# Kernel tuning notes

Hardware: AMD Instinct MI355X
Metric: run time of the kernel (lower is better)

Reference implementation:

```python
import jax, jax.numpy as jnp
import numpy as np

D_MODEL = 768
N_HEADS = 12
D_HEAD = D_MODEL // N_HEADS


def setup_inputs() -> dict:
    key = jax.random.key(0)
    k_x, k_qw, k_qb, k_ow, k_ob = jax.random.split(key, 5)
    B, N = 2, 4096
    scale = 1.0 / np.sqrt(D_MODEL)
    return {
        "x": jax.random.normal(k_x, (B, N, D_MODEL), dtype=jnp.float32),
        # torch nn.Linear stores weight as [out_features, in_features]
        "qkv_w": jax.random.uniform(k_qw, (3 * D_MODEL, D_MODEL), jnp.float32, -scale, scale),
        "qkv_b": jax.random.uniform(k_qb, (3 * D_MODEL,), jnp.float32, -scale, scale),
        "out_w": jax.random.uniform(k_ow, (D_MODEL, D_MODEL), jnp.float32, -scale, scale),
        "out_b": jax.random.uniform(k_ob, (D_MODEL,), jnp.float32, -scale, scale),
    }


def reference(x, qkv_w, qkv_b, out_w, out_b):
    B, N, D = x.shape
    qkv = x @ qkv_w.T + qkv_b                                   # [B, N, 3D]
    qkv = qkv.reshape(B, N, 3, N_HEADS, D_HEAD)
    qkv = jnp.transpose(qkv, (2, 0, 3, 1, 4))                    # [3, B, H, N, d]
    q, k, v = qkv[0], qkv[1], qkv[2]
    scores = jnp.einsum("bhqd,bhkd->bhqk", q, k) / np.sqrt(D_HEAD)
    attn = jax.nn.softmax(scores, axis=-1)
    out = jnp.einsum("bhqk,bhkd->bhqd", attn, v)                 # [B, H, N, d]
    out = jnp.transpose(out, (0, 2, 1, 3)).reshape(B, N, D)
    return out @ out_w.T + out_b
```

## Files before the change

### kernel.cpp

```cpp
#include <hip/hip_runtime.h>
#include <cstdint>

#define SEQ 4096
#define NH 12
#define DH 64
#define DM 768
#define MT 8192
#define QKVN 2304

typedef __bf16 bf16;
typedef __attribute__((ext_vector_type(8))) __bf16 bf16x8;
typedef __attribute__((ext_vector_type(4))) __bf16 bf16x4;
typedef __attribute__((ext_vector_type(2))) __bf16 bf16x2;
typedef __attribute__((ext_vector_type(4))) float f32x4;
typedef __attribute__((ext_vector_type(16))) float f32x16;
typedef __attribute__((ext_vector_type(2))) int int2v;

__device__ __forceinline__ void async_ld16(const void* g, void* lds) {
  __builtin_amdgcn_global_load_lds(
      (__attribute__((address_space(1))) void*)(void*)g,
      (__attribute__((address_space(3))) void*)lds, 16, 0, 0);
}

__device__ __forceinline__ int sexp2_bits(float s) {
  return (int)__builtin_fmaf(s, 8388608.0f, 1065091072.0f);
}

__device__ __forceinline__ int pack_hi16(int lo, int hi) {
#if __has_builtin(__builtin_amdgcn_perm)
  return (int)__builtin_amdgcn_perm((unsigned)hi, (unsigned)lo, 0x07060302u);
#else
  return (int)(((unsigned)lo >> 16) | ((unsigned)hi & 0xffff0000u));
#endif
}

__device__ __forceinline__ void lane32_swap(int& a, int& b) {
#if __has_builtin(__builtin_amdgcn_permlane32_swap)
  int2v r = __builtin_amdgcn_permlane32_swap(a, b, false, false);
  a = r.x; b = r.y;
#else
  int hi = (threadIdx.x & 63) >> 5;
  int ra = __shfl_xor(a, 32, 64), rb = __shfl_xor(b, 32, 64);
  int na = hi ? rb : a;
  int nb = hi ? b : ra;
  a = na; b = nb;
#endif
}

#define NX4  (MT * DM / 4)
#define NW14 (QKVN * DM / 4)
#define NW24 (DM * DM / 4)
__global__ void cvt_all(const float* __restrict__ x, const float* __restrict__ w1,
                        const float* __restrict__ w2, bf16* __restrict__ xb,
                        bf16* __restrict__ wb1, bf16* __restrict__ wb2) {
  int i = blockIdx.x * blockDim.x + threadIdx.x;
  const float* src; bf16* dst; int j;
  if (i < NX4) { src = x; dst = xb; j = i; }
  else if (i < NX4 + NW14) { src = w1; dst = wb1; j = i - NX4; }
  else if (i < NX4 + NW14 + NW24) { src = w2; dst = wb2; j = i - NX4 - NW14; }
  else return;
  f32x4 v = ((const f32x4*)src)[j];
  bf16x4 o;
  o.x = (bf16)v.x; o.y = (bf16)v.y; o.z = (bf16)v.z; o.w = (bf16)v.w;
  ((bf16x4*)dst)[j] = o;
}

template<int MODE>
__global__ __launch_bounds__(256) void gemm_bt(
    const bf16* __restrict__ A, const bf16* __restrict__ Bw,
    const float* __restrict__ bias,
    bf16* __restrict__ outQ, bf16* __restrict__ outK, bf16* __restrict__ outVt,
    float* __restrict__ outF,
    int M, int N, int K)
{
  __shared__ bf16 smem[2 * 128 * 64];
  bf16* sA = smem;
  bf16* sB = smem + 128 * 64;
  bf16* sT = smem;

  const int tid  = threadIdx.x;
  const int wave = tid >> 6;
  const int lane = tid & 63;
  const int l15  = lane & 15;
  const int quad = lane >> 4;

  constexpr int NT = (MODE == 0) ? (QKVN / 128) : (DM / 128);
  const int lin = blockIdx.x;
  const int rem = lin % (NT * 8);
  const int m0 = ((lin / (NT * 8)) * 8 + (rem % 8)) * 128;
  const int n0 = (rem / 8) * 128;

  const int rowbase = (wave >> 1) * 64;
  const int colbase = (wave & 1) * 64;

  f32x4 acc[4][4] = {};

  const int srow = lane >> 3;
  const int spg  = (lane & 7) ^ srow;
  const int xk   = l15 & 7;

  for (int kt = 0; kt < K; kt += 64) {
#pragma unroll
    for (int p = 0; p < 8; ++p) {
      int chunk = p * 4 + wave;
      if (chunk < 16) {
        int row = chunk * 8 + srow;
        async_ld16(A + (size_t)(m0 + row) * K + kt + spg * 8, &sA[chunk * 512]);
      } else {
        int row = (chunk - 16) * 8 + srow;
        async_ld16(Bw + (size_t)(n0 + row) * K + kt + spg * 8, &sB[(chunk - 16) * 512]);
      }
    }
    __syncthreads();

#pragma unroll
    for (int ks = 0; ks < 2; ++ks) {
      bf16x8 af[4], bfr[4];
#pragma unroll
      for (int rt = 0; rt < 4; ++rt)
        af[rt] = *(const bf16x8*)&sA[(rowbase + rt * 16 + l15) * 64 +
                                     (((ks * 4 + quad) ^ xk) * 8)];
#pragma unroll
      for (int ct = 0; ct < 4; ++ct)
        bfr[ct] = *(const bf16x8*)&sB[(colbase + ct * 16 + l15) * 64 +
                                      (((ks * 4 + quad) ^ xk) * 8)];
#pragma unroll
      for (int rt = 0; rt < 4; ++rt)
#pragma unroll
        for (int ct = 0; ct < 4; ++ct)
          acc[rt][ct] = __builtin_amdgcn_mfma_f32_16x16x32_bf16(af[rt], bfr[ct], acc[rt][ct], 0, 0, 0);
    }
    __syncthreads();
  }

  if (MODE == 0) {
    const int g = n0 / DM;
    if (g < 2) {
      const float qscale = 0.125f * 1.4426950408889634f;
#pragma unroll
      for (int ct = 0; ct < 4; ++ct) {
        int j = n0 + colbase + ct * 16 + l15;
        float bj = bias[j];
        int f = j % DM;
        int h = f >> 6, d = f & 63;
#pragma unroll
        for (int rt = 0; rt < 4; ++rt) {
          int mrow = m0 + rowbase + rt * 16 + quad * 4;
#pragma unroll
          for (int r = 0; r < 4; ++r) {
            float v = acc[rt][ct][r] + bj;
            int m = mrow + r;
            int b = m >> 12, n = m & 4095;
            int bh = b * NH + h;
            if (g == 0) outQ[((size_t)bh * SEQ + n) * DH + d] = (bf16)(v * qscale);
            else        outK[((size_t)bh * SEQ + n) * DH + d] = (bf16)v;
          }
        }
      }
    } else {
      const int f0 = n0 - 2 * DM;
      const int b = m0 >> 12, n0m = m0 & 4095;
#pragma unroll
      for (int p = 0; p < 2; ++p) {
        __syncthreads();
        if (colbase == p * 64) {
#pragma unroll
          for (int ct = 0; ct < 4; ++ct) {
            int jl = ct * 16 + l15;
            float bj = bias[n0 + p * 64 + jl];
#pragma unroll
            for (int rt = 0; rt < 4; ++rt) {
              int ml = rowbase + rt * 16 + quad * 4;
#pragma unroll
              for (int r = 0; r < 4; ++r)
                sT[jl * 136 + ml + r] = (bf16)(acc[rt][ct][r] + bj);
            }
          }
        }
        __syncthreads();
#pragma unroll
        for (int p2 = 0; p2 < 4; ++p2) {
          int slot = p2 * 256 + tid;
          int jr = slot >> 4, mc = (slot & 15) * 8;
          int fj = f0 + p * 64 + jr;
          int h = fj >> 6, d = fj & 63;
          *(bf16x8*)&outVt[((size_t)(b * NH + h) * DH + d) * SEQ + n0m + mc] =
              *(const bf16x8*)&sT[jr * 136 + mc];
        }
      }
    }
  } else {
#pragma unroll
    for (int ct = 0; ct < 4; ++ct) {
      int j = n0 + colbase + ct * 16 + l15;
      float bj = bias[j];
#pragma unroll
      for (int rt = 0; rt < 4; ++rt) {
        int mrow = m0 + rowbase + rt * 16 + quad * 4;
#pragma unroll
        for (int r = 0; r < 4; ++r)
          outF[(size_t)(mrow + r) * N + j] = acc[rt][ct][r] + bj;
      }
    }
  }
}

#define SOFTPV(S, R0, R1, R2, R3, OA, OB) do {                               \
    int b0 = sexp2_bits(S[8*kc+0]); int b1 = sexp2_bits(S[8*kc+1]);          \
    int b2 = sexp2_bits(S[8*kc+2]); int b3 = sexp2_bits(S[8*kc+3]);          \
    int b4 = sexp2_bits(S[8*kc+4]); int b5 = sexp2_bits(S[8*kc+5]);          \
    int b6 = sexp2_bits(S[8*kc+6]); int b7 = sexp2_bits(S[8*kc+7]);          \
    R0 += __int_as_float(b0 & 0xffff0000) + __int_as_float(b4 & 0xffff0000); \
    R1 += __int_as_float(b1 & 0xffff0000) + __int_as_float(b5 & 0xffff0000); \
    R2 += __int_as_float(b2 & 0xffff0000) + __int_as_float(b6 & 0xffff0000); \
    R3 += __int_as_float(b3 & 0xffff0000) + __int_as_float(b7 & 0xffff0000); \
    int g0a = pack_hi16(b0, b1), g0b = pack_hi16(b2, b3);                    \
    int g1a = pack_hi16(b4, b5), g1b = pack_hi16(b6, b7);                    \
    lane32_swap(g0a, g1a); lane32_swap(g0b, g1b);                            \
    union { int i[4]; bf16x8 v; } Af_;                                       \
    Af_.i[0] = g0a; Af_.i[1] = g0b; Af_.i[2] = g1a; Af_.i[3] = g1b;          \
    OA = __builtin_amdgcn_mfma_f32_32x32x16_bf16(Af_.v, vf0, OA, 0, 0, 0);   \
    OB = __builtin_amdgcn_mfma_f32_32x32x16_bf16(Af_.v, vf1, OB, 0, 0, 0);   \
  } while (0)

__global__ __launch_bounds__(256, 2) void flash_attn(
    const bf16* __restrict__ Q, const bf16* __restrict__ Kg,
    const bf16* __restrict__ Vt, bf16* __restrict__ Oout)
{
  __shared__ bf16 sK[2][64 * 64];
  __shared__ bf16 sV[2][64 * 64];

  const int L    = blockIdx.x + (SEQ / 256) * blockIdx.y;
  const int xcd  = L & 7;
  const int slot = L >> 3;
  const int bh   = xcd + 8 * (slot >> 4);
  const int qb   = slot & 15;

  {
    int ph = (qb + bh) & 3;
    if (ph == 1) __builtin_amdgcn_s_sleep(2);
    else if (ph == 2) __builtin_amdgcn_s_sleep(4);
    else if (ph == 3) __builtin_amdgcn_s_sleep(6);
  }

  const int tid  = threadIdx.x;
  const int wave = tid >> 6;
  const int lane = tid & 63;
  const int l31  = lane & 31;
  const int hi   = lane >> 5;
  const int q0w  = qb * 256 + wave * 64;

  const bf16* Qb = Q  + (size_t)bh * SEQ * DH;
  const bf16* Kb = Kg + (size_t)bh * SEQ * DH;
  const bf16* Vb = Vt + (size_t)bh * DH * SEQ;

  const int srow = lane >> 3;
  const int spg  = lane & 7;

  bf16x8 qf0[4], qf1[4];
#pragma unroll
  for (int dc = 0; dc < 4; ++dc) {
    qf0[dc] = *(const bf16x8*)&Qb[(size_t)(q0w + l31) * DH + dc * 16 + hi * 8];
    qf1[dc] = *(const bf16x8*)&Qb[(size_t)(q0w + 32 + l31) * DH + dc * 16 + hi * 8];
  }

  f32x16 o00 = {}, o01 = {}, o10 = {}, o11 = {};
  float r00 = 0.f, r01 = 0.f, r02 = 0.f, r03 = 0.f;
  float r10 = 0.f, r11 = 0.f, r12 = 0.f, r13 = 0.f;

  const int keyk = (l31 & 7) ^ (((l31 >> 3) & 3) << 1);
  int off[4];
#pragma unroll
  for (int dc = 0; dc < 4; ++dc)
    off[dc] = l31 * 64 + (((dc * 2 + hi) ^ keyk) * 8);

  auto stage = [&](int kt, int buf) {
#pragma unroll
    for (int j = 0; j < 2; ++j) {
      int r0 = wave * 16 + j * 8;
      int row = r0 + srow;
      int lg = spg ^ (row & 7) ^ (((row >> 3) & 3) << 1);
      async_ld16(Kb + (size_t)(kt + row) * DH + lg * 8, &sK[buf][r0 * 64]);
      async_ld16(Vb + (size_t)row * SEQ + kt + lg * 8, &sV[buf][r0 * 64]);
    }
  };

  auto compute = [&](const bf16* sKp, const bf16* sVp) {
#pragma unroll
    for (int kb = 0; kb < 2; ++kb) {
      bf16x8 kf[4];
#pragma unroll
      for (int dc = 0; dc < 4; ++dc)
        kf[dc] = *(const bf16x8*)&sKp[off[dc] + kb * 2048];
      f32x16 s0 = {}, s1 = {};
#pragma unroll
      for (int dc = 0; dc < 4; ++dc) {
        s0 = __builtin_amdgcn_mfma_f32_32x32x16_bf16(kf[dc], qf0[dc], s0, 0, 0, 0);
        s1 = __builtin_amdgcn_mfma_f32_32x32x16_bf16(kf[dc], qf1[dc], s1, 0, 0, 0);
      }
#pragma unroll
      for (int kc = 0; kc < 2; ++kc) {
        bf16x8 vf0 = *(const bf16x8*)&sVp[off[kb * 2 + kc]];
        bf16x8 vf1 = *(const bf16x8*)&sVp[off[kb * 2 + kc] + 2048];
        SOFTPV(s0, r00, r01, r02, r03, o00, o01);
        SOFTPV(s1, r10, r11, r12, r13, o10, o11);
      }
    }
  };

  stage(0, 0);
  __syncthreads();

  for (int kt = 0; kt < SEQ; kt += 128) {
    if (kt + 64 < SEQ) stage(kt + 64, 1);
    compute(sK[0], sV[0]);
    __syncthreads();
    if (kt + 128 < SEQ) stage(kt + 128, 0);
    compute(sK[1], sV[1]);
    __syncthreads();
  }

  float rsum0 = (r00 + r01) + (r02 + r03);
  rsum0 += __shfl_xor(rsum0, 32, 64);
  float inv0 = 1.0f / rsum0;
  float rsum1 = (r10 + r11) + (r12 + r13);
  rsum1 += __shfl_xor(rsum1, 32, 64);
  float inv1 = 1.0f / rsum1;

  const int bg = bh / NH, h = bh % NH;
#pragma unroll
  for (int i = 0; i < 16; ++i) {
    int ql = 8 * (i >> 2) + (i & 3) + 4 * hi;
    float iva = __shfl(inv0, ql, 64);
    size_t basea = (size_t)(bg * SEQ + q0w + ql) * DM + h * DH;
    Oout[basea + l31]      = (bf16)(o00[i] * iva);
    Oout[basea + 32 + l31] = (bf16)(o01[i] * iva);
    float ivb = __shfl(inv1, ql, 64);
    size_t baseb = (size_t)(bg * SEQ + q0w + 32 + ql) * DM + h * DH;
    Oout[baseb + l31]      = (bf16)(o10[i] * ivb);
    Oout[baseb + 32 + l31] = (bf16)(o11[i] * ivb);
  }
}

extern "C" void kernel_launch(void* const* d_in, const int* in_sizes, int n_in,
                              void* d_out, int out_size, void* d_ws, size_t ws_size,
                              hipStream_t stream) {
  const float* x     = (const float*)d_in[0];
  const float* qkv_w = (const float*)d_in[1];
  const float* qkv_b = (const float*)d_in[2];
  const float* out_w = (const float*)d_in[3];
  const float* out_b = (const float*)d_in[4];
  float* out = (float*)d_out;

  char* w = (char*)d_ws;
  bf16* xb    = (bf16*)w; w += (size_t)MT * DM * 2;
  bf16* wqkv  = (bf16*)w; w += (size_t)QKVN * DM * 2;
  bf16* wout  = (bf16*)w; w += (size_t)DM * DM * 2;
  bf16* Qw    = (bf16*)w; w += (size_t)MT * DM * 2;
  bf16* Kw    = (bf16*)w; w += (size_t)MT * DM * 2;
  bf16* Vtw   = (bf16*)w; w += (size_t)MT * DM * 2;
  bf16* attnV = (bf16*)w; w += (size_t)MT * DM * 2;

  const int tot4 = NX4 + NW14 + NW24;
  cvt_all<<<dim3((tot4 + 255) / 256), 256, 0, stream>>>(x, qkv_w, out_w, xb, wqkv, wout);

  gemm_bt<0><<<dim3((QKVN / 128) * (MT / 128)), 256, 0, stream>>>(
      xb, wqkv, qkv_b, Qw, Kw, Vtw, nullptr, MT, QKVN, DM);

  flash_attn<<<dim3(SEQ / 256, 2 * NH), 256, 0, stream>>>(Qw, Kw, Vtw, attnV);

  gemm_bt<1><<<dim3((DM / 128) * (MT / 128)), 256, 0, stream>>>(
      attnV, wout, out_b, nullptr, nullptr, nullptr, out, MT, DM, DM);
}
```

Measured before the change: 283.8 us.

## Split attention key range in two with fp32 partials and a merge kernel

Flash attention now splits each query block's key sequence into two halves, doubling the grid from 384 to 768 blocks. Each half writes unnormalized fp32 outputs and row sums to workspace, and a new merge kernel adds them, normalizes and writes bf16. Launch bounds move to 3 blocks per CU and the first QK MFMA starts from a constant zero accumulator. This trades extra global traffic (about 50MB of fp32 partials) and one more launch for better CU occupancy and load balance. The old path remains as a fallback when the workspace is too small.

```diff
diff --git a/kernel.cpp b/kernel.cpp
--- a/kernel.cpp
+++ b/kernel.cpp
@@ -7,6 +7,7 @@
 #define DM 768
 #define MT 8192
 #define QKVN 2304
+#define BH 24
 
 typedef __bf16 bf16;
 typedef __attribute__((ext_vector_type(8))) __bf16 bf16x8;
@@ -223,21 +224,32 @@
     OB = __builtin_amdgcn_mfma_f32_32x32x16_bf16(Af_.v, vf1, OB, 0, 0, 0);   \
   } while (0)
 
-__global__ __launch_bounds__(256, 2) void flash_attn(
+template<int SPLIT>
+__global__ __launch_bounds__(256, 3) void flash_attn(
     const bf16* __restrict__ Q, const bf16* __restrict__ Kg,
-    const bf16* __restrict__ Vt, bf16* __restrict__ Oout)
+    const bf16* __restrict__ Vt, float* __restrict__ Op,
+    float* __restrict__ Rs, bf16* __restrict__ Oout)
 {
   __shared__ bf16 sK[2][64 * 64];
   __shared__ bf16 sV[2][64 * 64];
 
-  const int L    = blockIdx.x + (SEQ / 256) * blockIdx.y;
-  const int xcd  = L & 7;
-  const int slot = L >> 3;
-  const int bh   = xcd + 8 * (slot >> 4);
-  const int qb   = slot & 15;
+  int bh, qb, kh;
+  if (SPLIT) {
+    const int L    = blockIdx.x + 32 * blockIdx.y;
+    const int slot = L >> 3;
+    bh = (L & 7) + 8 * (slot >> 5);
+    qb = (slot & 31) >> 1;
+    kh = slot & 1;
+  } else {
+    const int L    = blockIdx.x + 16 * blockIdx.y;
+    const int slot = L >> 3;
+    bh = (L & 7) + 8 * (slot >> 4);
+    qb = slot & 15;
+    kh = 0;
+  }
 
   {
-    int ph = (qb + bh) & 3;
+    int ph = (qb + bh + kh) & 3;
     if (ph == 1) __builtin_amdgcn_s_sleep(2);
     else if (ph == 2) __builtin_amdgcn_s_sleep(4);
     else if (ph == 3) __builtin_amdgcn_s_sleep(6);
@@ -249,6 +261,8 @@
   const int l31  = lane & 31;
   const int hi   = lane >> 5;
   const int q0w  = qb * 256 + wave * 64;
+  const int kbase = SPLIT ? kh * (SEQ / 2) : 0;
+  const int kend  = SPLIT ? kbase + SEQ / 2 : SEQ;
 
   const bf16* Qb = Q  + (size_t)bh * SEQ * DH;
   const bf16* Kb = Kg + (size_t)bh * SEQ * DH;
@@ -265,6 +279,7 @@
   }
 
   f32x16 o00 = {}, o01 = {}, o10 = {}, o11 = {};
+  const f32x16 zc = {};
   float r00 = 0.f, r01 = 0.f, r02 = 0.f, r03 = 0.f;
   float r10 = 0.f, r11 = 0.f, r12 = 0.f, r13 = 0.f;
 
@@ -292,9 +307,10 @@
 #pragma unroll
       for (int dc = 0; dc < 4; ++dc)
         kf[dc] = *(const bf16x8*)&sKp[off[dc] + kb * 2048];
-      f32x16 s0 = {}, s1 = {};
-#pragma unroll
-      for (int dc = 0; dc < 4; ++dc) {
+      f32x16 s0 = __builtin_amdgcn_mfma_f32_32x32x16_bf16(kf[0], qf0[0], zc, 0, 0, 0);
+      f32x16 s1 = __builtin_amdgcn_mfma_f32_32x32x16_bf16(kf[0], qf1[0], zc, 0, 0, 0);
+#pragma unroll
+      for (int dc = 1; dc < 4; ++dc) {
         s0 = __builtin_amdgcn_mfma_f32_32x32x16_bf16(kf[dc], qf0[dc], s0, 0, 0, 0);
         s1 = __builtin_amdgcn_mfma_f32_32x32x16_bf16(kf[dc], qf1[dc], s1, 0, 0, 0);
       }
@@ -308,38 +324,75 @@
     }
   };
 
-  stage(0, 0);
+  stage(kbase, 0);
   __syncthreads();
 
-  for (int kt = 0; kt < SEQ; kt += 128) {
-    if (kt + 64 < SEQ) stage(kt + 64, 1);
+  for (int kt = kbase; kt < kend; kt += 128) {
+    if (kt + 64 < kend) stage(kt + 64, 1);
     compute(sK[0], sV[0]);
     __syncthreads();
-    if (kt + 128 < SEQ) stage(kt + 128, 0);
+    if (kt + 128 < kend) stage(kt + 128, 0);
     compute(sK[1], sV[1]);
     __syncthreads();
   }
 
   float rsum0 = (r00 + r01) + (r02 + r03);
   rsum0 += __shfl_xor(rsum0, 32, 64);
-  float inv0 = 1.0f / rsum0;
   float rsum1 = (r10 + r11) + (r12 + r13);
   rsum1 += __shfl_xor(rsum1, 32, 64);
-  float inv1 = 1.0f / rsum1;
-
-  const int bg = bh / NH, h = bh % NH;
-#pragma unroll
-  for (int i = 0; i < 16; ++i) {
-    int ql = 8 * (i >> 2) + (i & 3) + 4 * hi;
-    float iva = __shfl(inv0, ql, 64);
-    size_t basea = (size_t)(bg * SEQ + q0w + ql) * DM + h * DH;
-    Oout[basea + l31]      = (bf16)(o00[i] * iva);
-    Oout[basea + 32 + l31] = (bf16)(o01[i] * iva);
-    float ivb = __shfl(inv1, ql, 64);
-    size_t baseb = (size_t)(bg * SEQ + q0w + 32 + ql) * DM + h * DH;
-    Oout[baseb + l31]      = (bf16)(o10[i] * ivb);
-    Oout[baseb + 32 + l31] = (bf16)(o11[i] * ivb);
-  }
+
+  if (SPLIT) {
+    float* Oh = Op + ((size_t)(kh * BH + bh) * SEQ + q0w) * DH;
+    if (hi == 0) {
+      float* Rh = Rs + (size_t)(kh * BH + bh) * SEQ + q0w;
+      Rh[l31]      = rsum0;
+      Rh[32 + l31] = rsum1;
+    }
+#pragma unroll
+    for (int i = 0; i < 16; ++i) {
+      int ql = 8 * (i >> 2) + (i & 3) + 4 * hi;
+      Oh[(size_t)ql * DH + l31]             = o00[i];
+      Oh[(size_t)ql * DH + 32 + l31]        = o01[i];
+      Oh[(size_t)(32 + ql) * DH + l31]      = o10[i];
+      Oh[(size_t)(32 + ql) * DH + 32 + l31] = o11[i];
+    }
+  } else {
+    float inv0 = 1.0f / rsum0;
+    float inv1 = 1.0f / rsum1;
+    const int bg = bh / NH, h = bh % NH;
+#pragma unroll
+    for (int i = 0; i < 16; ++i) {
+      int ql = 8 * (i >> 2) + (i & 3) + 4 * hi;
+      float iva = __shfl(inv0, ql, 64);
+      size_t basea = (size_t)(bg * SEQ + q0w + ql) * DM + h * DH;
+      Oout[basea + l31]      = (bf16)(o00[i] * iva);
+      Oout[basea + 32 + l31] = (bf16)(o01[i] * iva);
+      float ivb = __shfl(inv1, ql, 64);
+      size_t baseb = (size_t)(bg * SEQ + q0w + 32 + ql) * DM + h * DH;
+      Oout[baseb + l31]      = (bf16)(o10[i] * ivb);
+      Oout[baseb + 32 + l31] = (bf16)(o11[i] * ivb);
+    }
+  }
+}
+
+__global__ __launch_bounds__(256) void merge_halves(
+    const float* __restrict__ Op, const float* __restrict__ Rs,
+    bf16* __restrict__ attnV)
+{
+  int i = blockIdx.x * 256 + threadIdx.x;
+  if (i >= BH * SEQ * (DH / 4)) return;
+  int dq = i & 15, row = i >> 4;
+  f32x4 a = ((const f32x4*)Op)[(size_t)row * 16 + dq];
+  f32x4 b = ((const f32x4*)Op)[((size_t)BH * SEQ + row) * 16 + dq];
+  float inv = 1.0f / (Rs[row] + Rs[BH * SEQ + row]);
+  int q = row & (SEQ - 1), bh = row >> 12;
+  int bg = bh / NH, h = bh % NH;
+  bf16x4 r;
+  r.x = (bf16)((a.x + b.x) * inv);
+  r.y = (bf16)((a.y + b.y) * inv);
+  r.z = (bf16)((a.z + b.z) * inv);
+  r.w = (bf16)((a.w + b.w) * inv);
+  *(bf16x4*)&attnV[((size_t)(bg * SEQ + q)) * DM + h * DH + dq * 4] = r;
 }
 
 extern "C" void kernel_launch(void* const* d_in, const int* in_sizes, int n_in,
@@ -360,6 +413,9 @@
   bf16* Kw    = (bf16*)w; w += (size_t)MT * DM * 2;
   bf16* Vtw   = (bf16*)w; w += (size_t)MT * DM * 2;
   bf16* attnV = (bf16*)w; w += (size_t)MT * DM * 2;
+  float* Opf  = (float*)w; w += (size_t)2 * BH * SEQ * DH * 4;
+  float* Rsf  = (float*)w; w += (size_t)2 * BH * SEQ * 4;
+  const size_t ws_need = (size_t)(w - (char*)d_ws);
 
   const int tot4 = NX4 + NW14 + NW24;
   cvt_all<<<dim3((tot4 + 255) / 256), 256, 0, stream>>>(x, qkv_w, out_w, xb, wqkv, wout);
@@ -367,7 +423,12 @@
   gemm_bt<0><<<dim3((QKVN / 128) * (MT / 128)), 256, 0, stream>>>(
       xb, wqkv, qkv_b, Qw, Kw, Vtw, nullptr, MT, QKVN, DM);
 
-  flash_attn<<<dim3(SEQ / 256, 2 * NH), 256, 0, stream>>>(Qw, Kw, Vtw, attnV);
+  if (ws_size >= ws_need) {
+    flash_attn<1><<<dim3(32, BH), 256, 0, stream>>>(Qw, Kw, Vtw, Opf, Rsf, nullptr);
+    merge_halves<<<dim3(BH * SEQ * (DH / 4) / 256), 256, 0, stream>>>(Opf, Rsf, attnV);
+  } else {
+    flash_attn<0><<<dim3(16, BH), 256, 0, stream>>>(Qw, Kw, Vtw, nullptr, nullptr, attnV);
+  }
 
   gemm_bt<1><<<dim3((DM / 128) * (MT / 128)), 256, 0, stream>>>(
       attnV, wout, out_b, nullptr, nullptr, nullptr, out, MT, DM, DM);
```

New measurement: 592.1 us. 2.09x slower.
